# Kernel tuning notes

Measured on AMD Instinct MI355X. Metric: run time of the kernel, lower is better.

## Reference

```python
import jax, jax.numpy as jnp
import numpy as np

B_, L_, D_, E_, N_, R_, K_ = 2, 2048, 2048, 4096, 16, 128, 4


def setup_inputs() -> dict:
    key = jax.random.key(0)
    ks = jax.random.split(key, 12)
    s = lambda k, shape, scale: jax.random.normal(k, shape, dtype=jnp.float32) * scale
    return {
        "resid": s(ks[0], (B_, L_, D_), 1.0),
        "norm_w": jnp.ones((D_,), jnp.float32),
        "W_skip": s(ks[1], (E_, D_), D_ ** -0.5),
        "W_in": s(ks[2], (E_, D_), D_ ** -0.5),
        "conv_w": s(ks[3], (E_, 1, K_), K_ ** -0.5),
        "conv_b": s(ks[4], (E_,), 0.02),
        "W_d1": s(ks[5], (R_, E_), E_ ** -0.5),
        "W_d2": s(ks[6], (E_, R_), R_ ** -0.5),
        "b_d2": s(ks[7], (E_,), 0.02) - 2.0,  # bias toward small delta like mamba dt init
        "W_Bm": s(ks[8], (N_, E_), E_ ** -0.5),
        "W_Cm": s(ks[9], (N_, E_), E_ ** -0.5),
        "A_log": s(ks[10], (E_, N_), 0.5),
        "W_D": jnp.ones((E_,), jnp.float32),
        "W_out": s(ks[11], (D_, E_), E_ ** -0.5),
    }


def reference(resid, norm_w, W_skip, W_in, conv_w, conv_b, W_d1, W_d2, b_d2,
              W_Bm, W_Cm, A_log, W_D, W_out):
    eps = 1e-5
    E, K = conv_w.shape[0], conv_w.shape[-1]
    # RMSNorm
    x = resid * jax.lax.rsqrt(jnp.mean(resid * resid, -1, keepdims=True) + eps) * norm_w
    skip = x @ W_skip.T                       # [B,L,E]
    x = x @ W_in.T                            # [B,L,E]
    # depthwise causal conv over L (torch pads both sides then cuts to L == left pad K-1)
    xc = jnp.swapaxes(x, 1, 2)                # [B,E,L]
    xc = jax.lax.conv_general_dilated(
        xc, conv_w, (1,), [(K - 1, 0)],
        dimension_numbers=("NCH", "OIH", "NCH"), feature_group_count=E)
    xc = xc + conv_b[None, :, None]
    x = jax.nn.silu(jnp.swapaxes(xc, 1, 2))   # [B,L,E] ssm input
    A = -jnp.exp(A_log)                       # [E,N]
    # input-dependent params, batched over B,L
    delta = jax.nn.softplus((x @ W_d1.T) @ W_d2.T + b_d2)  # [B,L,E]
    Bt = x @ W_Bm.T                           # [B,L,N]
    Ct = x @ W_Cm.T                           # [B,L,N]

    def step(h, inp):
        x_t, d_t, b_t, c_t = inp              # [B,E],[B,E],[B,N],[B,N]
        h = jnp.exp(d_t[:, :, None] * A) * h + (d_t * x_t)[:, :, None] * b_t[:, None, :]
        y = jnp.einsum("ben,bn->be", h, c_t)
        return h, y

    xs = (jnp.swapaxes(x, 0, 1), jnp.swapaxes(delta, 0, 1),
          jnp.swapaxes(Bt, 0, 1), jnp.swapaxes(Ct, 0, 1))
    h0 = jnp.zeros((x.shape[0], A.shape[0], A.shape[1]), x.dtype)
    _, ys = jax.lax.scan(step, h0, xs)        # [L,B,E]
    y = jnp.swapaxes(ys, 0, 1)                # [B,L,E]
    y = y + x * W_D
    y = y * jax.nn.silu(skip)
    return resid + y @ W_out.T
```

## Files before the change

kernel.cpp:

```cpp
#include <hip/hip_runtime.h>
#include <hip/hip_bf16.h>
#include <math.h>

#define MB_ 4096
#define DD_ 2048
#define EE_ 4096
#define LL_ 2048
#define NN_ 16
#define RR_ 128
#define CH_ 16
#define LCH_ (LL_ / CH_)

using short8  = __attribute__((ext_vector_type(8))) short;
using floatx4 = __attribute__((ext_vector_type(4))) float;
typedef unsigned short ushort_t;

__device__ __forceinline__ float bf2f(ushort_t u) {
    unsigned int x = ((unsigned int)u) << 16;
    return __builtin_bit_cast(float, x);
}
__device__ __forceinline__ ushort_t f2bf(float f) {
    unsigned int x = __builtin_bit_cast(unsigned int, f);
    unsigned int lsb = (x >> 16) & 1u;
    x += 0x7fffu + lsb;
    return (ushort_t)(x >> 16);
}
__device__ __forceinline__ float bf_lo(unsigned int u) {
    return __builtin_bit_cast(float, u << 16);
}
__device__ __forceinline__ float bf_hi(unsigned int u) {
    return __builtin_bit_cast(float, u & 0xffff0000u);
}

__device__ __forceinline__ void gld16(const ushort_t* g, ushort_t* l) {
    __builtin_amdgcn_global_load_lds(
        (const __attribute__((address_space(1))) unsigned int*)g,
        (__attribute__((address_space(3))) unsigned int*)l,
        16, 0, 0);
}

typedef __attribute__((address_space(3))) const ushort_t* lds_cptr;
__device__ __forceinline__ short8 dsr128(const ushort_t* p) {
    short8 d;
    asm volatile("ds_read_b128 %0, %1" : "=&v"(d) : "v"((lds_cptr)p));
    return d;
}

__global__ __launch_bounds__(256) void cvt_bf16_k(const float* __restrict__ src,
                                                  ushort_t* __restrict__ dst, int n4) {
    int i = blockIdx.x * 256 + threadIdx.x;
    if (i >= n4) return;
    float4 v = ((const float4*)src)[i];
    ushort_t* d = dst + (size_t)i * 4;
    d[0] = f2bf(v.x); d[1] = f2bf(v.y); d[2] = f2bf(v.z); d[3] = f2bf(v.w);
}

__global__ __launch_bounds__(256) void pack_bcd1_k(const float* __restrict__ Wb,
                                                   const float* __restrict__ Wc,
                                                   const float* __restrict__ Wd1,
                                                   ushort_t* __restrict__ dst) {
    int i = blockIdx.x * 256 + threadIdx.x;
    int row = i >> 10;
    int c4  = i & 1023;
    float4 v;
    if (row < 16)       v = ((const float4*)(Wb  + (size_t)row       * 4096))[c4];
    else if (row < 32)  v = ((const float4*)(Wc  + (size_t)(row - 16)* 4096))[c4];
    else if (row < 160) v = ((const float4*)(Wd1 + (size_t)(row - 32)* 4096))[c4];
    else { v.x = 0.f; v.y = 0.f; v.z = 0.f; v.w = 0.f; }
    ushort_t* d = dst + (size_t)i * 4;
    d[0] = f2bf(v.x); d[1] = f2bf(v.y); d[2] = f2bf(v.z); d[3] = f2bf(v.w);
}

__global__ __launch_bounds__(256) void rmsnorm_k(const float* __restrict__ resid,
                                                 const float* __restrict__ nw,
                                                 ushort_t* __restrict__ xn) {
    __shared__ float red[4];
    int row = blockIdx.x;
    int tid = threadIdx.x;
    const float* rp = resid + (size_t)row * DD_;
    float4 a = ((const float4*)rp)[tid];
    float4 b = ((const float4*)rp)[tid + 256];
    float ss = a.x*a.x + a.y*a.y + a.z*a.z + a.w*a.w
             + b.x*b.x + b.y*b.y + b.z*b.z + b.w*b.w;
    #pragma unroll
    for (int off = 32; off; off >>= 1) ss += __shfl_xor(ss, off);
    int wave = tid >> 6;
    if ((tid & 63) == 0) red[wave] = ss;
    __syncthreads();
    float total = red[0] + red[1] + red[2] + red[3];
    float scale = rsqrtf(total * (1.0f / (float)DD_) + 1e-5f);
    ushort_t* op = xn + (size_t)row * DD_;
    int i0 = tid * 4;
    op[i0+0] = f2bf(a.x * scale * nw[i0+0]);
    op[i0+1] = f2bf(a.y * scale * nw[i0+1]);
    op[i0+2] = f2bf(a.z * scale * nw[i0+2]);
    op[i0+3] = f2bf(a.w * scale * nw[i0+3]);
    int i1 = (tid + 256) * 4;
    op[i1+0] = f2bf(b.x * scale * nw[i1+0]);
    op[i1+1] = f2bf(b.y * scale * nw[i1+1]);
    op[i1+2] = f2bf(b.z * scale * nw[i1+2]);
    op[i1+3] = f2bf(b.w * scale * nw[i1+3]);
}

#define GMODE_BF16     0
#define GMODE_F32      1
#define GMODE_SOFTPLUS 2
#define GMODE_RESID    3

__global__ __launch_bounds__(256) void gemm_bt(
    const ushort_t* __restrict__ A, const ushort_t* __restrict__ Bw,
    int lda, int ldb, int K,
    void* __restrict__ outp, int ldc, int ncols,
    const float* __restrict__ aux, int mode)
{
    __shared__ __align__(16) ushort_t As[128 * 64];
    __shared__ __align__(16) ushort_t Bs[128 * 64];
    const int tid  = threadIdx.x;
    const int lane = tid & 63;
    const int wave = tid >> 6;
    const int quad = lane >> 4;
    const int l16  = lane & 15;
    const int mb   = (wave & 1) * 64;
    const int nb   = (wave >> 1) * 64;
    const int tileM = blockIdx.y * 128;
    const int tileN = blockIdx.x * 128;

    const int srow = wave * 8 + (lane >> 3);
    const int sq   = ((lane & 7) - (srow >> 1)) & 7;
    const ushort_t* Ag = A  + (size_t)(tileM + srow) * lda + sq * 8;
    const ushort_t* Bg = Bw + (size_t)(tileN + srow) * ldb + sq * 8;
    ushort_t* AsD = As + wave * 512;
    ushort_t* BsD = Bs + wave * 512;

    floatx4 acc[4][4];
    #pragma unroll
    for (int i = 0; i < 4; i++)
        #pragma unroll
        for (int j = 0; j < 4; j++)
            acc[i][j] = (floatx4){0.f, 0.f, 0.f, 0.f};

    int aoff[4][2], boff[4][2];
    #pragma unroll
    for (int i = 0; i < 4; i++) {
        int ar = mb + i * 16 + l16;
        int br = nb + i * 16 + l16;
        #pragma unroll
        for (int kk = 0; kk < 2; kk++) {
            aoff[i][kk] = ar * 64 + (((kk * 4 + quad) + (ar >> 1)) & 7) * 8;
            boff[i][kk] = br * 64 + (((kk * 4 + quad) + (br >> 1)) & 7) * 8;
        }
    }

    for (int kb = 0; kb < K; kb += 64) {
        __syncthreads();
        #pragma unroll
        for (int i = 0; i < 4; i++) {
            gld16(Ag + (size_t)i * 32 * lda + kb, AsD + i * 2048);
            gld16(Bg + (size_t)i * 32 * ldb + kb, BsD + i * 2048);
        }
        __syncthreads();
        #pragma unroll
        for (int kk = 0; kk < 2; kk++) {
            short8 af[4], bfr[4];
            #pragma unroll
            for (int i = 0; i < 4; i++)
                af[i] = *(const short8*)(As + aoff[i][kk]);
            #pragma unroll
            for (int j = 0; j < 4; j++)
                bfr[j] = *(const short8*)(Bs + boff[j][kk]);
            #pragma unroll
            for (int i = 0; i < 4; i++)
                #pragma unroll
                for (int j = 0; j < 4; j++)
                    acc[i][j] = __builtin_amdgcn_mfma_f32_16x16x32_bf16(af[i], bfr[j], acc[i][j], 0, 0, 0);
        }
    }

    #pragma unroll
    for (int i = 0; i < 4; i++) {
        #pragma unroll
        for (int j = 0; j < 4; j++) {
            int col = tileN + nb + j * 16 + l16;
            if (col >= ncols) continue;
            int rowb = tileM + mb + i * 16 + quad * 4;
            #pragma unroll
            for (int r = 0; r < 4; r++) {
                size_t idx = (size_t)(rowb + r) * ldc + col;
                float v = acc[i][j][r];
                if (mode == GMODE_BF16) {
                    ((ushort_t*)outp)[idx] = f2bf(v);
                } else if (mode == GMODE_F32) {
                    ((float*)outp)[idx] = v;
                } else if (mode == GMODE_SOFTPLUS) {
                    float z = v + aux[col];
                    float sp = (z > 20.f) ? z : log1pf(expf(z));
                    ((ushort_t*)outp)[idx] = f2bf(sp);
                } else {
                    ((float*)outp)[idx] = v + aux[idx];
                }
            }
        }
    }
}

__global__ __launch_bounds__(256) void gemm_db(
    const ushort_t* __restrict__ A, const ushort_t* __restrict__ Bw,
    int lda, int ldb, int K,
    void* __restrict__ outp, int ldc, int ncols,
    const float* __restrict__ aux, int mode)
{
    __shared__ __align__(16) ushort_t As[2][128 * 64];
    __shared__ __align__(16) ushort_t Bs[2][128 * 64];
    const int tid  = threadIdx.x;
    const int lane = tid & 63;
    const int wave = tid >> 6;
    const int quad = lane >> 4;
    const int l16  = lane & 15;
    const int mb   = (wave & 1) * 64;
    const int nb   = (wave >> 1) * 64;
    const int tileM = blockIdx.y * 128;
    const int tileN = blockIdx.x * 128;

    const int srow = wave * 8 + (lane >> 3);
    const int sq   = ((lane & 7) - (srow >> 1)) & 7;
    const ushort_t* Ag = A  + (size_t)(tileM + srow) * lda + sq * 8;
    const ushort_t* Bg = Bw + (size_t)(tileN + srow) * ldb + sq * 8;
    const int sdst = wave * 512;

    floatx4 acc[4][4];
    #pragma unroll
    for (int i = 0; i < 4; i++)
        #pragma unroll
        for (int j = 0; j < 4; j++)
            acc[i][j] = (floatx4){0.f, 0.f, 0.f, 0.f};

    int aoff[4][2], boff[4][2];
    #pragma unroll
    for (int i = 0; i < 4; i++) {
        int ar = mb + i * 16 + l16;
        int br = nb + i * 16 + l16;
        #pragma unroll
        for (int kk = 0; kk < 2; kk++) {
            aoff[i][kk] = ar * 64 + (((kk * 4 + quad) + (ar >> 1)) & 7) * 8;
            boff[i][kk] = br * 64 + (((kk * 4 + quad) + (br >> 1)) & 7) * 8;
        }
    }

    const int NT = K >> 6;

    #pragma unroll
    for (int i = 0; i < 4; i++) {
        gld16(Ag + (size_t)i * 32 * lda, &As[0][sdst + i * 2048]);
        gld16(Bg + (size_t)i * 32 * ldb, &Bs[0][sdst + i * 2048]);
    }
    asm volatile("s_waitcnt vmcnt(0)" ::: "memory");
    __syncthreads();

    for (int t = 0; t < NT; ++t) {
        const int cur = t & 1;
        if (t + 1 < NT) {
            const int kb = (t + 1) << 6;
            #pragma unroll
            for (int i = 0; i < 4; i++) {
                gld16(Ag + (size_t)i * 32 * lda + kb, &As[cur ^ 1][sdst + i * 2048]);
                gld16(Bg + (size_t)i * 32 * ldb + kb, &Bs[cur ^ 1][sdst + i * 2048]);
            }
        }
        #pragma unroll
        for (int kk = 0; kk < 2; kk++) {
            short8 af[4], bfr[4];
            #pragma unroll
            for (int i = 0; i < 4; i++)
                af[i] = dsr128(&As[cur][aoff[i][kk]]);
            #pragma unroll
            for (int j = 0; j < 4; j++)
                bfr[j] = dsr128(&Bs[cur][boff[j][kk]]);
            asm volatile("s_waitcnt lgkmcnt(0)" ::: "memory");
            __builtin_amdgcn_sched_barrier(0);
            #pragma unroll
            for (int i = 0; i < 4; i++)
                #pragma unroll
                for (int j = 0; j < 4; j++)
                    acc[i][j] = __builtin_amdgcn_mfma_f32_16x16x32_bf16(af[i], bfr[j], acc[i][j], 0, 0, 0);
        }
        asm volatile("s_waitcnt vmcnt(0)" ::: "memory");
        __syncthreads();
    }

    #pragma unroll
    for (int i = 0; i < 4; i++) {
        #pragma unroll
        for (int j = 0; j < 4; j++) {
            int col = tileN + nb + j * 16 + l16;
            if (col >= ncols) continue;
            int rowb = tileM + mb + i * 16 + quad * 4;
            #pragma unroll
            for (int r = 0; r < 4; r++) {
                size_t idx = (size_t)(rowb + r) * ldc + col;
                float v = acc[i][j][r];
                if (mode == GMODE_BF16) {
                    ((ushort_t*)outp)[idx] = f2bf(v);
                } else if (mode == GMODE_F32) {
                    ((float*)outp)[idx] = v;
                } else if (mode == GMODE_SOFTPLUS) {
                    float z = v + aux[col];
                    float sp = (z > 20.f) ? z : log1pf(expf(z));
                    ((ushort_t*)outp)[idx] = f2bf(sp);
                } else {
                    ((float*)outp)[idx] = v + aux[idx];
                }
            }
        }
    }
}

__global__ __launch_bounds__(256) void conv_silu_k(const ushort_t* __restrict__ xin,
                                                   const float* __restrict__ cw,
                                                   const float* __restrict__ cb,
                                                   ushort_t* __restrict__ xs) {
    int e  = blockIdx.x * 256 + threadIdx.x;
    int l0 = blockIdx.y * 4;
    int b  = blockIdx.z;
    float w0 = cw[e * 4 + 0], w1 = cw[e * 4 + 1], w2 = cw[e * 4 + 2], w3 = cw[e * 4 + 3];
    float bias = cb[e];
    const ushort_t* p = xin + ((size_t)(b * LL_ + l0)) * EE_ + e;
    ushort_t*       o = xs  + ((size_t)(b * LL_ + l0)) * EE_ + e;
    float v[7];
    #pragma unroll
    for (int j = 0; j < 7; j++) {
        int l = l0 + j - 3;
        v[j] = (l >= 0) ? bf2f(p[(ptrdiff_t)(j - 3) * EE_]) : 0.f;
    }
    #pragma unroll
    for (int r = 0; r < 4; r++) {
        float s = bias + v[r] * w0 + v[r+1] * w1 + v[r+2] * w2 + v[r+3] * w3;
        float out = s / (1.f + expf(-s));
        o[(size_t)r * EE_] = f2bf(out);
    }
}

__global__ __launch_bounds__(256) void scan1_k(
    const ushort_t* __restrict__ xs, const ushort_t* __restrict__ delta,
    const ushort_t* __restrict__ bc, const float* __restrict__ A_log,
    float* __restrict__ P, float* __restrict__ S)
{
    const int e = blockIdx.x * 256 + threadIdx.x;
    const int c = blockIdx.y;
    const int b = blockIdx.z;
    const int l0 = c * LCH_;

    float acoef[NN_];
    {
        const float4* ap = (const float4*)(A_log + (size_t)e * NN_);
        #pragma unroll
        for (int k = 0; k < 4; k++) {
            float4 v = ap[k];
            acoef[k*4+0] = -expf(v.x) * 1.44269504f;
            acoef[k*4+1] = -expf(v.y) * 1.44269504f;
            acoef[k*4+2] = -expf(v.z) * 1.44269504f;
            acoef[k*4+3] = -expf(v.w) * 1.44269504f;
        }
    }

    const size_t m0 = (size_t)(b * LL_ + l0);
    const ushort_t* dp  = delta + m0 * EE_ + e;
    const ushort_t* xp  = xs    + m0 * EE_ + e;
    const ushort_t* bcp = bc    + m0 * 160;

    float h[NN_];
    #pragma unroll
    for (int n = 0; n < NN_; n++) h[n] = 0.f;
    float sd = 0.f;

    for (int l = 0; l < LCH_; ++l) {
        float dlt = bf2f(*dp); dp += EE_;
        float xv  = bf2f(*xp); xp += EE_;
        unsigned int q[4];
        *(uint4*)q = *(const uint4*)(bcp);
        unsigned int q2[4];
        *(uint4*)q2 = *(const uint4*)(bcp + 8);
        bcp += 160;
        sd += dlt;
        float dx = dlt * xv;
        float Bn[NN_];
        #pragma unroll
        for (int k = 0; k < 4; k++) {
            Bn[k*2+0] = bf_lo(q[k]);  Bn[k*2+1] = bf_hi(q[k]);
            Bn[8+k*2] = bf_lo(q2[k]); Bn[9+k*2] = bf_hi(q2[k]);
        }
        #pragma unroll
        for (int n = 0; n < NN_; n++) {
            float a = exp2f(dlt * acoef[n]);
            h[n] = fmaf(a, h[n], dx * Bn[n]);
        }
    }

    const size_t ob = (((size_t)(b * CH_ + c)) * EE_ + e) * NN_;
    float4* Pp = (float4*)(P + ob);
    float4* Sp = (float4*)(S + ob);
    #pragma unroll
    for (int k = 0; k < 4; k++) {
        float4 pv, sv;
        pv.x = exp2f(acoef[k*4+0] * sd); pv.y = exp2f(acoef[k*4+1] * sd);
        pv.z = exp2f(acoef[k*4+2] * sd); pv.w = exp2f(acoef[k*4+3] * sd);
        sv.x = h[k*4+0]; sv.y = h[k*4+1]; sv.z = h[k*4+2]; sv.w = h[k*4+3];
        Pp[k] = pv; Sp[k] = sv;
    }
}

__global__ __launch_bounds__(256) void scan2_k(const float* __restrict__ P, float* S) {
    int idx = blockIdx.x * 256 + threadIdx.x;
    int b  = idx >> 16;
    int en = idx & 65535;
    size_t base = ((size_t)b * CH_) * (EE_ * NN_) + en;
    float h = 0.f;
    #pragma unroll
    for (int c = 0; c < CH_; c++) {
        size_t o = base + (size_t)c * (EE_ * NN_);
        float Pv = P[o];
        float Sv = S[o];
        S[o] = h;
        h = fmaf(Pv, h, Sv);
    }
}

__global__ __launch_bounds__(256) void scan3_k(
    const ushort_t* __restrict__ xs, const ushort_t* delta,
    const ushort_t* __restrict__ bc, const ushort_t* __restrict__ skip,
    const float* __restrict__ A_log, const float* __restrict__ WD,
    const float* __restrict__ S, ushort_t* ys)
{
    const int e = blockIdx.x * 256 + threadIdx.x;
    const int c = blockIdx.y;
    const int b = blockIdx.z;
    const int l0 = c * LCH_;

    float acoef[NN_];
    {
        const float4* ap = (const float4*)(A_log + (size_t)e * NN_);
        #pragma unroll
        for (int k = 0; k < 4; k++) {
            float4 v = ap[k];
            acoef[k*4+0] = -expf(v.x) * 1.44269504f;
            acoef[k*4+1] = -expf(v.y) * 1.44269504f;
            acoef[k*4+2] = -expf(v.z) * 1.44269504f;
            acoef[k*4+3] = -expf(v.w) * 1.44269504f;
        }
    }
    const float wd = WD[e];

    float h[NN_];
    {
        const float4* Sp = (const float4*)(S + (((size_t)(b * CH_ + c)) * EE_ + e) * NN_);
        #pragma unroll
        for (int k = 0; k < 4; k++) {
            float4 v = Sp[k];
            h[k*4+0] = v.x; h[k*4+1] = v.y; h[k*4+2] = v.z; h[k*4+3] = v.w;
        }
    }

    const size_t m0 = (size_t)(b * LL_ + l0);
    const ushort_t* dp  = delta + m0 * EE_ + e;
    const ushort_t* xp  = xs    + m0 * EE_ + e;
    const ushort_t* sp  = skip  + m0 * EE_ + e;
    const ushort_t* bcp = bc    + m0 * 160;
    ushort_t*       yp  = ys    + m0 * EE_ + e;

    for (int l = 0; l < LCH_; ++l) {
        float dlt = bf2f(*dp); dp += EE_;
        float xv  = bf2f(*xp); xp += EE_;
        float sk  = bf2f(*sp); sp += EE_;
        unsigned int q[8];
        *(uint4*)(q)     = *(const uint4*)(bcp);
        *(uint4*)(q + 4) = *(const uint4*)(bcp + 8);
        unsigned int r[8];
        *(uint4*)(r)     = *(const uint4*)(bcp + 16);
        *(uint4*)(r + 4) = *(const uint4*)(bcp + 24);
        bcp += 160;
        float dx = dlt * xv;
        float y = 0.f;
        #pragma unroll
        for (int k = 0; k < 8; k++) {
            float B0 = bf_lo(q[k]), B1 = bf_hi(q[k]);
            float C0 = bf_lo(r[k]), C1 = bf_hi(r[k]);
            float a0 = exp2f(dlt * acoef[k*2+0]);
            float a1 = exp2f(dlt * acoef[k*2+1]);
            h[k*2+0] = fmaf(a0, h[k*2+0], dx * B0);
            h[k*2+1] = fmaf(a1, h[k*2+1], dx * B1);
            y = fmaf(h[k*2+0], C0, y);
            y = fmaf(h[k*2+1], C1, y);
        }
        y = (y + xv * wd) * (sk / (1.f + expf(-sk)));
        *yp = f2bf(y); yp += EE_;
    }
}

extern "C" void kernel_launch(void* const* d_in, const int* in_sizes, int n_in,
                              void* d_out, int out_size, void* d_ws, size_t ws_size,
                              hipStream_t stream) {
    const float* resid  = (const float*)d_in[0];
    const float* norm_w = (const float*)d_in[1];
    const float* W_skip = (const float*)d_in[2];
    const float* W_in   = (const float*)d_in[3];
    const float* conv_w = (const float*)d_in[4];
    const float* conv_b = (const float*)d_in[5];
    const float* W_d1   = (const float*)d_in[6];
    const float* W_d2   = (const float*)d_in[7];
    const float* b_d2   = (const float*)d_in[8];
    const float* W_Bm   = (const float*)d_in[9];
    const float* W_Cm   = (const float*)d_in[10];
    const float* A_log  = (const float*)d_in[11];
    const float* W_D    = (const float*)d_in[12];
    const float* W_out  = (const float*)d_in[13];
    float* out = (float*)d_out;

    const size_t MB16 = (size_t)16 * 1024 * 1024;
    const size_t MB32 = (size_t)32 * 1024 * 1024;
    char* w = (char*)d_ws;
    ushort_t* xn     = (ushort_t*)w;
    float*    Pbuf   = (float*)w;
    ushort_t* woutb  = (ushort_t*)w;
    w += MB16;
    ushort_t* wbuf   = (ushort_t*)w;
    ushort_t* wbcd1b = wbuf;
    ushort_t* wd2b   = wbuf + (size_t)256 * EE_;
    ushort_t* bcd1b  = wd2b + (size_t)EE_ * RR_;
    float*    Sbuf   = (float*)(bcd1b + (size_t)MB_ * 160);
    w += MB16;
    ushort_t* skipb  = (ushort_t*)w; w += MB32;
    ushort_t* xinb   = (ushort_t*)w;
    ushort_t* deltab = xinb;
    ushort_t* ysb    = xinb;
    w += MB32;
    ushort_t* xsb    = (ushort_t*)w; w += MB32;

    rmsnorm_k<<<MB_, 256, 0, stream>>>(resid, norm_w, xn);

    cvt_bf16_k<<<8192, 256, 0, stream>>>(W_skip, wbuf, (EE_ * DD_) / 4);
    gemm_db<<<dim3(EE_ / 128, MB_ / 128), 256, 0, stream>>>(
        xn, wbuf, DD_, DD_, DD_, skipb, EE_, EE_, nullptr, GMODE_BF16);

    cvt_bf16_k<<<8192, 256, 0, stream>>>(W_in, wbuf, (EE_ * DD_) / 4);
    gemm_db<<<dim3(EE_ / 128, MB_ / 128), 256, 0, stream>>>(
        xn, wbuf, DD_, DD_, DD_, xinb, EE_, EE_, nullptr, GMODE_BF16);

    pack_bcd1_k<<<1024, 256, 0, stream>>>(W_Bm, W_Cm, W_d1, wbcd1b);
    cvt_bf16_k<<<512, 256, 0, stream>>>(W_d2, wd2b, (EE_ * RR_) / 4);

    conv_silu_k<<<dim3(EE_ / 256, LL_ / 4, 2), 256, 0, stream>>>(xinb, conv_w, conv_b, xsb);

    gemm_bt<<<dim3(2, MB_ / 128), 256, 0, stream>>>(
        xsb, wbcd1b, EE_, EE_, EE_, bcd1b, 160, 160, nullptr, GMODE_BF16);

    gemm_bt<<<dim3(EE_ / 128, MB_ / 128), 256, 0, stream>>>(
        bcd1b + 32, wd2b, 160, RR_, RR_, deltab, EE_, EE_, b_d2, GMODE_SOFTPLUS);

    scan1_k<<<dim3(EE_ / 256, CH_, 2), 256, 0, stream>>>(
        xsb, deltab, bcd1b, A_log, Pbuf, Sbuf);
    scan2_k<<<(2 * EE_ * NN_) / 256, 256, 0, stream>>>(Pbuf, Sbuf);
    scan3_k<<<dim3(EE_ / 256, CH_, 2), 256, 0, stream>>>(
        xsb, deltab, bcd1b, skipb, A_log, W_D, Sbuf, ysb);

    cvt_bf16_k<<<8192, 256, 0, stream>>>(W_out, woutb, (DD_ * EE_) / 4);
    gemm_db<<<dim3(DD_ / 128, MB_ / 128), 256, 0, stream>>>(
        ysb, woutb, EE_, EE_, EE_, out, DD_, DD_, resid, GMODE_RESID);
}
```

Measured before the change: 900.3 us.

## Split SSM state dimension across four lanes per channel in scan kernels

```diff
diff --git a/kernel.cpp b/kernel.cpp
--- a/kernel.cpp
+++ b/kernel.cpp
@@ -344,68 +344,49 @@
     const ushort_t* __restrict__ bc, const float* __restrict__ A_log,
     float* __restrict__ P, float* __restrict__ S)
 {
-    const int e = blockIdx.x * 256 + threadIdx.x;
+    const int tid = threadIdx.x;
+    const int ns  = tid & 3;
+    const int e   = blockIdx.x * 64 + (tid >> 2);
     const int c = blockIdx.y;
     const int b = blockIdx.z;
     const int l0 = c * LCH_;
 
-    float acoef[NN_];
+    float acoef[4];
     {
-        const float4* ap = (const float4*)(A_log + (size_t)e * NN_);
-        #pragma unroll
-        for (int k = 0; k < 4; k++) {
-            float4 v = ap[k];
-            acoef[k*4+0] = -expf(v.x) * 1.44269504f;
-            acoef[k*4+1] = -expf(v.y) * 1.44269504f;
-            acoef[k*4+2] = -expf(v.z) * 1.44269504f;
-            acoef[k*4+3] = -expf(v.w) * 1.44269504f;
-        }
+        float4 v = *(const float4*)(A_log + (size_t)e * NN_ + ns * 4);
+        acoef[0] = -expf(v.x) * 1.44269504f;
+        acoef[1] = -expf(v.y) * 1.44269504f;
+        acoef[2] = -expf(v.z) * 1.44269504f;
+        acoef[3] = -expf(v.w) * 1.44269504f;
     }
 
     const size_t m0 = (size_t)(b * LL_ + l0);
     const ushort_t* dp  = delta + m0 * EE_ + e;
     const ushort_t* xp  = xs    + m0 * EE_ + e;
-    const ushort_t* bcp = bc    + m0 * 160;
-
-    float h[NN_];
-    #pragma unroll
-    for (int n = 0; n < NN_; n++) h[n] = 0.f;
+    const ushort_t* bcp = bc    + m0 * 160 + ns * 4;
+
+    float h[4] = {0.f, 0.f, 0.f, 0.f};
     float sd = 0.f;
 
     for (int l = 0; l < LCH_; ++l) {
         float dlt = bf2f(*dp); dp += EE_;
         float xv  = bf2f(*xp); xp += EE_;
-        unsigned int q[4];
-        *(uint4*)q = *(const uint4*)(bcp);
-        unsigned int q2[4];
-        *(uint4*)q2 = *(const uint4*)(bcp + 8);
-        bcp += 160;
+        uint2 q = *(const uint2*)(bcp); bcp += 160;
         sd += dlt;
         float dx = dlt * xv;
-        float Bn[NN_];
-        #pragma unroll
-        for (int k = 0; k < 4; k++) {
-            Bn[k*2+0] = bf_lo(q[k]);  Bn[k*2+1] = bf_hi(q[k]);
-            Bn[8+k*2] = bf_lo(q2[k]); Bn[9+k*2] = bf_hi(q2[k]);
-        }
-        #pragma unroll
-        for (int n = 0; n < NN_; n++) {
-            float a = exp2f(dlt * acoef[n]);
-            h[n] = fmaf(a, h[n], dx * Bn[n]);
-        }
-    }
-
-    const size_t ob = (((size_t)(b * CH_ + c)) * EE_ + e) * NN_;
-    float4* Pp = (float4*)(P + ob);
-    float4* Sp = (float4*)(S + ob);
-    #pragma unroll
-    for (int k = 0; k < 4; k++) {
-        float4 pv, sv;
-        pv.x = exp2f(acoef[k*4+0] * sd); pv.y = exp2f(acoef[k*4+1] * sd);
-        pv.z = exp2f(acoef[k*4+2] * sd); pv.w = exp2f(acoef[k*4+3] * sd);
-        sv.x = h[k*4+0]; sv.y = h[k*4+1]; sv.z = h[k*4+2]; sv.w = h[k*4+3];
-        Pp[k] = pv; Sp[k] = sv;
-    }
+        float Bn[4] = { bf_lo(q.x), bf_hi(q.x), bf_lo(q.y), bf_hi(q.y) };
+        #pragma unroll
+        for (int n = 0; n < 4; n++)
+            h[n] = fmaf(exp2f(dlt * acoef[n]), h[n], dx * Bn[n]);
+    }
+
+    const size_t ob = (((size_t)(b * CH_ + c)) * EE_ + e) * NN_ + ns * 4;
+    float4 pv, sv;
+    pv.x = exp2f(acoef[0] * sd); pv.y = exp2f(acoef[1] * sd);
+    pv.z = exp2f(acoef[2] * sd); pv.w = exp2f(acoef[3] * sd);
+    sv.x = h[0]; sv.y = h[1]; sv.z = h[2]; sv.w = h[3];
+    *(float4*)(P + ob) = pv;
+    *(float4*)(S + ob) = sv;
 }
 
 __global__ __launch_bounds__(256) void scan2_k(const float* __restrict__ P, float* S) {
@@ -430,33 +411,27 @@
     const float* __restrict__ A_log, const float* __restrict__ WD,
     const float* __restrict__ S, ushort_t* ys)
 {
-    const int e = blockIdx.x * 256 + threadIdx.x;
+    const int tid = threadIdx.x;
+    const int ns  = tid & 3;
+    const int e   = blockIdx.x * 64 + (tid >> 2);
     const int c = blockIdx.y;
     const int b = blockIdx.z;
     const int l0 = c * LCH_;
 
-    float acoef[NN_];
+    float acoef[4];
     {
-        const float4* ap = (const float4*)(A_log + (size_t)e * NN_);
-        #pragma unroll
-        for (int k = 0; k < 4; k++) {
-            float4 v = ap[k];
-            acoef[k*4+0] = -expf(v.x) * 1.44269504f;
-            acoef[k*4+1] = -expf(v.y) * 1.44269504f;
-            acoef[k*4+2] = -expf(v.z) * 1.44269504f;
-            acoef[k*4+3] = -expf(v.w) * 1.44269504f;
-        }
+        float4 v = *(const float4*)(A_log + (size_t)e * NN_ + ns * 4);
+        acoef[0] = -expf(v.x) * 1.44269504f;
+        acoef[1] = -expf(v.y) * 1.44269504f;
+        acoef[2] = -expf(v.z) * 1.44269504f;
+        acoef[3] = -expf(v.w) * 1.44269504f;
     }
     const float wd = WD[e];
 
-    float h[NN_];
+    float h[4];
     {
-        const float4* Sp = (const float4*)(S + (((size_t)(b * CH_ + c)) * EE_ + e) * NN_);
-        #pragma unroll
-        for (int k = 0; k < 4; k++) {
-            float4 v = Sp[k];
-            h[k*4+0] = v.x; h[k*4+1] = v.y; h[k*4+2] = v.z; h[k*4+3] = v.w;
-        }
+        float4 v = *(const float4*)(S + (((size_t)(b * CH_ + c)) * EE_ + e) * NN_ + ns * 4);
+        h[0] = v.x; h[1] = v.y; h[2] = v.z; h[3] = v.w;
     }
 
     const size_t m0 = (size_t)(b * LL_ + l0);
@@ -470,28 +445,25 @@
         float dlt = bf2f(*dp); dp += EE_;
         float xv  = bf2f(*xp); xp += EE_;
         float sk  = bf2f(*sp); sp += EE_;
-        unsigned int q[8];
-        *(uint4*)(q)     = *(const uint4*)(bcp);
-        *(uint4*)(q + 4) = *(const uint4*)(bcp + 8);
-        unsigned int r[8];
-        *(uint4*)(r)     = *(const uint4*)(bcp + 16);
-        *(uint4*)(r + 4) = *(const uint4*)(bcp + 24);
+        uint2 qB = *(const uint2*)(bcp + ns * 4);
+        uint2 qC = *(const uint2*)(bcp + 16 + ns * 4);
         bcp += 160;
         float dx = dlt * xv;
+        float Bn[4] = { bf_lo(qB.x), bf_hi(qB.x), bf_lo(qB.y), bf_hi(qB.y) };
+        float Cn[4] = { bf_lo(qC.x), bf_hi(qC.x), bf_lo(qC.y), bf_hi(qC.y) };
         float y = 0.f;
         #pragma unroll
-        for (int k = 0; k < 8; k++) {
-            float B0 = bf_lo(q[k]), B1 = bf_hi(q[k]);
-            float C0 = bf_lo(r[k]), C1 = bf_hi(r[k]);
-            float a0 = exp2f(dlt * acoef[k*2+0]);
-            float a1 = exp2f(dlt * acoef[k*2+1]);
-            h[k*2+0] = fmaf(a0, h[k*2+0], dx * B0);
-            h[k*2+1] = fmaf(a1, h[k*2+1], dx * B1);
-            y = fmaf(h[k*2+0], C0, y);
-            y = fmaf(h[k*2+1], C1, y);
-        }
-        y = (y + xv * wd) * (sk / (1.f + expf(-sk)));
-        *yp = f2bf(y); yp += EE_;
+        for (int n = 0; n < 4; n++) {
+            h[n] = fmaf(exp2f(dlt * acoef[n]), h[n], dx * Bn[n]);
+            y = fmaf(h[n], Cn[n], y);
+        }
+        y += __shfl_xor(y, 1);
+        y += __shfl_xor(y, 2);
+        if (ns == 0) {
+            y = (y + xv * wd) * (sk / (1.f + expf(-sk)));
+            *yp = f2bf(y);
+        }
+        yp += EE_;
     }
 }
 
@@ -555,10 +527,10 @@
     gemm_bt<<<dim3(EE_ / 128, MB_ / 128), 256, 0, stream>>>(
         bcd1b + 32, wd2b, 160, RR_, RR_, deltab, EE_, EE_, b_d2, GMODE_SOFTPLUS);
 
-    scan1_k<<<dim3(EE_ / 256, CH_, 2), 256, 0, stream>>>(
+    scan1_k<<<dim3(EE_ / 64, CH_, 2), 256, 0, stream>>>(
         xsb, deltab, bcd1b, A_log, Pbuf, Sbuf);
     scan2_k<<<(2 * EE_ * NN_) / 256, 256, 0, stream>>>(Pbuf, Sbuf);
-    scan3_k<<<dim3(EE_ / 256, CH_, 2), 256, 0, stream>>>(
+    scan3_k<<<dim3(EE_ / 64, CH_, 2), 256, 0, stream>>>(
         xsb, deltab, bcd1b, skipb, A_log, W_D, Sbuf, ysb);
 
     cvt_bf16_k<<<8192, 256, 0, stream>>>(W_out, woutb, (DD_ * EE_) / 4);
```

Result: slower. 967.1 us (+7.4%).
